# Performance work log

Measured on AMD Instinct MI355X. Metric: run time of the kernel, lower is better.

## Reference

```python
import jax, jax.numpy as jnp
import numpy as np

N_NODES = 50000
N_EDGES = 800000
NFEAT = 128
NHID = 64  # gc1: NFEAT -> 2*NHID, gc2: 2*NHID -> NHID


def setup_inputs() -> dict:
    key = jax.random.key(0)
    k1, k2, k3, k4, k5 = jax.random.split(key, 5)
    feat = jax.random.normal(k1, (N_NODES, NFEAT), dtype=jnp.float32)
    src = jax.random.randint(k2, (N_EDGES,), 0, N_NODES, dtype=jnp.int32)
    dst = jax.random.randint(k3, (N_EDGES,), 0, N_NODES, dtype=jnp.int32)
    # GraphConv weights: (in_feats, out_feats), xavier-like scale
    W1 = jax.random.normal(k4, (NFEAT, 2 * NHID), dtype=jnp.float32) / np.sqrt(NFEAT)
    b1 = jnp.zeros((2 * NHID,), dtype=jnp.float32)
    W2 = jax.random.normal(k5, (2 * NHID, NHID), dtype=jnp.float32) / np.sqrt(2 * NHID)
    b2 = jnp.zeros((NHID,), dtype=jnp.float32)
    return {"feat": feat, "src": src, "dst": dst, "W1": W1, "b1": b1, "W2": W2, "b2": b2}


def _graph_conv(feat, src, dst, W, b):
    """DGL GraphConv, norm='both', allow_zero_in_degree=True.
    h = D_in^{-1/2} A (D_out^{-1/2} x) W + b, with degrees clamped to >= 1.
    Applies W before aggregation when in_feats > out_feats (saves bandwidth)."""
    N = feat.shape[0]
    ones = jnp.ones(src.shape[0], dtype=feat.dtype)
    deg_out = jnp.clip(jax.ops.segment_sum(ones, src, num_segments=N), 1.0)
    deg_in = jnp.clip(jax.ops.segment_sum(ones, dst, num_segments=N), 1.0)
    h = feat * (deg_out ** -0.5)[:, None]
    mult_first = W.shape[0] > W.shape[1]
    if mult_first:
        h = h @ W
    agg = jax.ops.segment_sum(h[src], dst, num_segments=N)  # [N, d]
    if not mult_first:
        agg = agg @ W
    return agg * (deg_in ** -0.5)[:, None] + b


def reference(feat, src, dst, W1, b1, W2, b2):
    x = jax.nn.relu(_graph_conv(feat, src, dst, W1, b1))
    # dropout is inactive in eval mode (F.dropout training=False)
    x = _graph_conv(x, src, dst, W2, b2)
    return jax.nn.log_softmax(x, axis=1)
```

## Files before the change

kernel.cpp:

```cpp
#include <hip/hip_runtime.h>
#include <math.h>


constexpr int NF   = 128;
constexpr int NH   = 64;
constexpr int CAP  = 48;
constexpr int EPB  = 4096;
constexpr int BCAP = 8192;
constexpr int NBKMAX = 256;
constexpr int CASTB = 192;

typedef unsigned int uint;
typedef unsigned short ushort_t;
typedef __attribute__((ext_vector_type(8))) short short8;
typedef __attribute__((ext_vector_type(4))) float f32x4;

__device__ __forceinline__ float bflo(uint u) { return __uint_as_float(u << 16); }
__device__ __forceinline__ float bfhi(uint u) { return __uint_as_float(u & 0xffff0000u); }
__device__ __forceinline__ uint packbf(float a, float b) {
    uint ua = __float_as_uint(a), ub = __float_as_uint(b);
    uint ra = (ua + 0x7fffu + ((ua >> 16) & 1u)) >> 16;
    uint rb = (ub + 0x7fffu + ((ub >> 16) & 1u)) >> 16;
    return ra | (rb << 16);
}
__device__ __forceinline__ ushort_t bf16u(float f) {
    uint u = __float_as_uint(f);
    return (ushort_t)((u + 0x7fffu + ((u >> 16) & 1u)) >> 16);
}
__device__ __forceinline__ short8 as_short8(uint4 u) {
    union { uint4 u; short8 s; } x; x.u = u; return x.s;
}

__global__ __launch_bounds__(1024) void partition_kernel(
        const int* __restrict__ src, const int* __restrict__ dst,
        uint* __restrict__ pairs_g, ushort_t* __restrict__ srcb_g,
        int* __restrict__ dcur, int* __restrict__ scur,
        const float* __restrict__ W1, const float* __restrict__ W2,
        uint* __restrict__ W1p, uint* __restrict__ W2p,
        const float* __restrict__ feat, uint* __restrict__ featb,
        int E, int nbk, int nchunk, int N) {
    if (blockIdx.x >= nchunk) {
        int xb = blockIdx.x - nchunk;
        if (xb < 12) {
            int i = xb * 1024 + threadIdx.x;
            if (i < 8192) {
                int jp = i & 3, g = (i >> 2) & 3, n = (i >> 4) & 127, kk = i >> 11;
                int k = kk * 32 + g * 8 + jp * 2;
                W1p[i] = packbf(W1[k * 128 + n], W1[(k + 1) * 128 + n]);
            } else if (i < 12288) {
                int j = i - 8192;
                int jp = j & 3, g = (j >> 2) & 3, n = (j >> 4) & 63, kk = j >> 10;
                int k = kk * 32 + g * 8 + jp * 2;
                W2p[j] = packbf(W2[k * 64 + n], W2[(k + 1) * 64 + n]);
            }
        } else {
            int items = N * 16;
            for (int k = (xb - 12) * 1024 + threadIdx.x; k < items; k += CASTB * 1024) {
                int r = k >> 4, ch = k & 15;
                const float4* f4 = (const float4*)(feat + (size_t)r * NF + ch * 8);
                float4 a = f4[0], c = f4[1];
                uint4 o;
                o.x = packbf(a.x, a.y);
                o.y = packbf(a.z, a.w);
                o.z = packbf(c.x, c.y);
                o.w = packbf(c.z, c.w);
                *(uint4*)(featb + (size_t)r * 64 + ch * 4) = o;
            }
        }
        return;
    }
    __shared__ uint     pl[EPB];
    __shared__ ushort_t sl[EPB];
    __shared__ int dh[NBKMAX], sh[NBKMAX];
    __shared__ int doff[NBKMAX], soff[NBKMAX];
    __shared__ int dbase[NBKMAX], sbase[NBKMAX];
    __shared__ int dpos[NBKMAX], spos[NBKMAX];
    int tid = threadIdx.x;
    int e0 = blockIdx.x * EPB;
    int ecnt = min(EPB, E - e0);
    int ecnt4 = ecnt >> 2;
    bool own = tid < ecnt4;
    int4 sR = make_int4(0, 0, 0, 0), dR = make_int4(0, 0, 0, 0);
    if (own) {
        sR = ((const int4*)(src + e0))[tid];
        dR = ((const int4*)(dst + e0))[tid];
    }

    for (int b = tid; b < nbk; b += 1024) { dh[b] = 0; sh[b] = 0; }
    __syncthreads();
    if (own) {
        atomicAdd(&dh[dR.x >> 8], 1); atomicAdd(&dh[dR.y >> 8], 1);
        atomicAdd(&dh[dR.z >> 8], 1); atomicAdd(&dh[dR.w >> 8], 1);
        atomicAdd(&sh[sR.x >> 8], 1); atomicAdd(&sh[sR.y >> 8], 1);
        atomicAdd(&sh[sR.z >> 8], 1); atomicAdd(&sh[sR.w >> 8], 1);
    }
    for (int i = ecnt4 * 4 + tid; i < ecnt; i += 1024) {
        atomicAdd(&dh[dst[e0 + i] >> 8], 1);
        atomicAdd(&sh[src[e0 + i] >> 8], 1);
    }
    __syncthreads();
    if (tid < 128) {
        int wv = tid >> 6, l = tid & 63, b0 = l * 4;
        const int* h = wv ? sh : dh;
        int* of      = wv ? soff : doff;
        int v0 = (b0     < nbk) ? h[b0]     : 0;
        int v1 = (b0 + 1 < nbk) ? h[b0 + 1] : 0;
        int v2 = (b0 + 2 < nbk) ? h[b0 + 2] : 0;
        int v3 = (b0 + 3 < nbk) ? h[b0 + 3] : 0;
        int lsum = v0 + v1 + v2 + v3;
        int sc = lsum;
        #pragma unroll
        for (int off = 1; off < 64; off <<= 1) {
            int t = __shfl_up(sc, off, 64);
            if (l >= off) sc += t;
        }
        int excl = sc - lsum;
        if (b0     < nbk) of[b0]     = excl;
        if (b0 + 1 < nbk) of[b0 + 1] = excl + v0;
        if (b0 + 2 < nbk) of[b0 + 2] = excl + v0 + v1;
        if (b0 + 3 < nbk) of[b0 + 3] = excl + v0 + v1 + v2;
    }
    for (int b = tid; b < nbk; b += 1024) {
        dbase[b] = atomicAdd(&dcur[b], dh[b]);
        sbase[b] = atomicAdd(&scur[b], sh[b]);
    }
    __syncthreads();
    for (int b = tid; b < nbk; b += 1024) { dpos[b] = doff[b]; spos[b] = soff[b]; }
    __syncthreads();
    if (own) {
        #pragma unroll
        for (int j = 0; j < 4; ++j) {
            int sj = (j == 0) ? sR.x : (j == 1) ? sR.y : (j == 2) ? sR.z : sR.w;
            int dj = (j == 0) ? dR.x : (j == 1) ? dR.y : (j == 2) ? dR.z : dR.w;
            int p = atomicAdd(&dpos[dj >> 8], 1);
            pl[p] = ((uint)sj << 16) | (uint)dj;
            int q = atomicAdd(&spos[sj >> 8], 1);
            sl[q] = (ushort_t)sj;
        }
    }
    for (int i = ecnt4 * 4 + tid; i < ecnt; i += 1024) {
        int s = src[e0 + i], d = dst[e0 + i];
        int p = atomicAdd(&dpos[d >> 8], 1);
        pl[p] = ((uint)s << 16) | (uint)d;
        int q = atomicAdd(&spos[s >> 8], 1);
        sl[q] = (ushort_t)s;
    }
    __syncthreads();
    if (own) {
        uint4 e4 = *(const uint4*)&pl[tid * 4];
        ushort4 s4 = *(const ushort4*)&sl[tid * 4];
        #pragma unroll
        for (int j = 0; j < 4; ++j) {
            uint e = (j == 0) ? e4.x : (j == 1) ? e4.y : (j == 2) ? e4.z : e4.w;
            int i = tid * 4 + j;
            int b = (int)((e & 0xffffu) >> 8);
            int gp = dbase[b] + (i - doff[b]);
            if (gp < BCAP) pairs_g[(size_t)b * BCAP + gp] = e;
            ushort_t sv = (j == 0) ? s4.x : (j == 1) ? s4.y : (j == 2) ? s4.z : s4.w;
            int b2 = (int)(sv >> 8);
            int gq = sbase[b2] + (i - soff[b2]);
            if (gq < BCAP) srcb_g[(size_t)b2 * BCAP + gq] = sv;
        }
    }
    for (int i = ecnt4 * 4 + tid; i < ecnt; i += 1024) {
        uint e = pl[i];
        int b = (int)((e & 0xffffu) >> 8);
        int gp = dbase[b] + (i - doff[b]);
        if (gp < BCAP) pairs_g[(size_t)b * BCAP + gp] = e;
        ushort_t sv = sl[i];
        int b2 = (int)(sv >> 8);
        int gq = sbase[b2] + (i - soff[b2]);
        if (gq < BCAP) srcb_g[(size_t)b2 * BCAP + gq] = sv;
    }
}

__global__ __launch_bounds__(1024) void bin_kernel(
        const uint* __restrict__ pairs_g, const ushort_t* __restrict__ srcb_g,
        const int* __restrict__ dcur, const int* __restrict__ scur,
        ushort_t* __restrict__ slots, int* __restrict__ lens,
        float* __restrict__ s_in, float* __restrict__ s_out, int N) {
    __shared__ ushort_t slots_l[256 * CAP];
    __shared__ int cin[256], cout[256];
    int tid = threadIdx.x;
    int b = blockIdx.x;
    int lo = b << 8;
    for (int r = tid; r < 256; r += 1024) { cin[r] = 0; cout[r] = 0; }
    __syncthreads();
    int dn = min(dcur[b], BCAP);
    for (int i = tid; i < dn; i += 1024) {
        uint e = pairs_g[(size_t)b * BCAP + i];
        int r = (int)(e & 255u);
        int p = atomicAdd(&cin[r], 1);
        if (p < CAP) slots_l[r * CAP + p] = (ushort_t)(e >> 16);
    }
    int sn = min(scur[b], BCAP);
    for (int i = tid; i < sn; i += 1024)
        atomicAdd(&cout[(int)srcb_g[(size_t)b * BCAP + i] - lo], 1);
    __syncthreads();
    int nrow = min(256, N - lo);
    {
        const uint4* sl4 = (const uint4*)slots_l;
        uint4* gs4 = (uint4*)(slots + (size_t)lo * CAP);
        int lim4 = nrow * (CAP / 8);
        for (int k = tid; k < 256 * CAP / 8; k += 1024)
            if (k < lim4) gs4[k] = sl4[k];
    }
    for (int r = tid; r < nrow; r += 1024) {
        int node = lo + r;
        int ci = cin[r];
        lens[node]  = min(ci, CAP);
        s_in[node]  = rsqrtf((float)max(ci, 1));
        s_out[node] = rsqrtf((float)max(cout[r], 1));
    }
}

__global__ __launch_bounds__(256) void agg1_kernel(const uint* __restrict__ featb,
        const int* __restrict__ lens, const ushort_t* __restrict__ slots,
        const float* __restrict__ s_out, uint* __restrict__ agg1b, int N) {
    int wave = threadIdx.x >> 6;
    int lane = threadIdx.x & 63;
    int q   = lane >> 4;
    int sub = lane & 15;
    int node = blockIdx.x * 4 + wave;
    if (node >= N) return;
    int beg = node * CAP;
    int len = lens[node];
    float acc[8] = {0.f, 0.f, 0.f, 0.f, 0.f, 0.f, 0.f, 0.f};
    if (len > 0) {
        int li = min(lane, len - 1);
        int sidx = (int)slots[beg + li];
        int quads = (len + 3) >> 2;
        #pragma unroll 4
        for (int k = 0; k < quads; ++k) {
            int e = 4 * k + q;
            int s = __shfl(sidx, e, 64);
            if (e < len) {
                float so = s_out[s];
                uint4 v = *(const uint4*)(featb + (size_t)s * 64 + sub * 4);
                acc[0] = fmaf(so, bflo(v.x), acc[0]);
                acc[1] = fmaf(so, bfhi(v.x), acc[1]);
                acc[2] = fmaf(so, bflo(v.y), acc[2]);
                acc[3] = fmaf(so, bfhi(v.y), acc[3]);
                acc[4] = fmaf(so, bflo(v.z), acc[4]);
                acc[5] = fmaf(so, bfhi(v.z), acc[5]);
                acc[6] = fmaf(so, bflo(v.w), acc[6]);
                acc[7] = fmaf(so, bfhi(v.w), acc[7]);
            }
        }
    }
    #pragma unroll
    for (int j = 0; j < 8; ++j) {
        acc[j] += __shfl_xor(acc[j], 32, 64);
        acc[j] += __shfl_xor(acc[j], 16, 64);
    }
    if (q == 0) {
        uint4 o;
        o.x = packbf(acc[0], acc[1]);
        o.y = packbf(acc[2], acc[3]);
        o.z = packbf(acc[4], acc[5]);
        o.w = packbf(acc[6], acc[7]);
        *(uint4*)(agg1b + (size_t)node * 64 + sub * 4) = o;
    }
}

__global__ __launch_bounds__(256) void fused_gemm_kernel(
        const uint* __restrict__ agg1b, const uint* __restrict__ W1p,
        const float* __restrict__ b1, const uint* __restrict__ W2p,
        const float* __restrict__ s_in, const float* __restrict__ s_out,
        uint* __restrict__ h2b, int N) {
    __shared__ ushort_t x1t[64][136];
    __shared__ float sin_l[64], sout_l[64];
    int t = threadIdx.x;
    int base = blockIdx.x * 64;
    int w    = t >> 6;
    int lane = t & 63;
    int c = lane & 15;
    int g = lane >> 4;

    if (t < 64)       sin_l[t]        = (base + t < N) ? s_in[base + t] : 0.f;
    else if (t < 128) sout_l[t - 64]  = (base + t - 64 < N) ? s_out[base + t - 64] : 0.f;
    __syncthreads();

    f32x4 zero = {0.f, 0.f, 0.f, 0.f};
    f32x4 c1[4][2];
    #pragma unroll
    for (int mt = 0; mt < 4; ++mt) { c1[mt][0] = zero; c1[mt][1] = zero; }
    #pragma unroll
    for (int kk = 0; kk < 4; ++kk) {
        short8 bf[2];
        #pragma unroll
        for (int ntl = 0; ntl < 2; ++ntl) {
            int n = (2 * w + ntl) * 16 + c;
            bf[ntl] = as_short8(*(const uint4*)(W1p + (size_t)kk * 2048 + n * 16 + g * 4));
        }
        #pragma unroll
        for (int mt = 0; mt < 4; ++mt) {
            int row = base + mt * 16 + c;
            short8 af = as_short8(*(const uint4*)(agg1b + (size_t)row * 64 + kk * 16 + g * 4));
            c1[mt][0] = __builtin_amdgcn_mfma_f32_16x16x32_bf16(af, bf[0], c1[mt][0], 0, 0, 0);
            c1[mt][1] = __builtin_amdgcn_mfma_f32_16x16x32_bf16(af, bf[1], c1[mt][1], 0, 0, 0);
        }
    }
    float bias0 = b1[(2 * w) * 16 + c];
    float bias1 = b1[(2 * w + 1) * 16 + c];
    #pragma unroll
    for (int mt = 0; mt < 4; ++mt) {
        #pragma unroll
        for (int r = 0; r < 4; ++r) {
            int rl = mt * 16 + g * 4 + r;
            float si = sin_l[rl], so = sout_l[rl];
            x1t[rl][(2 * w) * 16 + c]     = bf16u(fmaxf(fmaf(si, c1[mt][0][r], bias0), 0.f) * so);
            x1t[rl][(2 * w + 1) * 16 + c] = bf16u(fmaxf(fmaf(si, c1[mt][1][r], bias1), 0.f) * so);
        }
    }
    __syncthreads();

    f32x4 c2[4];
    #pragma unroll
    for (int mt = 0; mt < 4; ++mt) c2[mt] = zero;
    #pragma unroll
    for (int kk = 0; kk < 4; ++kk) {
        int n = w * 16 + c;
        short8 bf2 = as_short8(*(const uint4*)(W2p + (size_t)kk * 1024 + n * 16 + g * 4));
        #pragma unroll
        for (int mt = 0; mt < 4; ++mt) {
            short8 af = *(const short8*)&x1t[mt * 16 + c][kk * 32 + g * 8];
            c2[mt] = __builtin_amdgcn_mfma_f32_16x16x32_bf16(af, bf2, c2[mt], 0, 0, 0);
        }
    }
    __syncthreads();

    ushort_t* h2t = &x1t[0][0];
    #pragma unroll
    for (int mt = 0; mt < 4; ++mt) {
        #pragma unroll
        for (int r = 0; r < 4; ++r) {
            int rl = mt * 16 + g * 4 + r;
            h2t[rl * 72 + w * 16 + c] = bf16u(c2[mt][r]);
        }
    }
    __syncthreads();
    int row = t >> 2, ch = t & 3;
    if (base + row < N) {
        uint4 v0 = *(const uint4*)(h2t + row * 72 + ch * 16);
        uint4 v1 = *(const uint4*)(h2t + row * 72 + ch * 16 + 8);
        *(uint4*)(h2b + (size_t)(base + row) * 32 + ch * 8)     = v0;
        *(uint4*)(h2b + (size_t)(base + row) * 32 + ch * 8 + 4) = v1;
    }
}

__global__ __launch_bounds__(256) void agg2_softmax_kernel(const uint* __restrict__ h2b,
        const int* __restrict__ lens, const ushort_t* __restrict__ slots,
        const float* __restrict__ s_in, const float* __restrict__ b2,
        float* __restrict__ out, int N) {
    int wave = threadIdx.x >> 6;
    int lane = threadIdx.x & 63;
    int oct = lane >> 3;
    int sub = lane & 7;
    int node = blockIdx.x * 4 + wave;
    if (node >= N) return;
    int beg = node * CAP;
    int len = lens[node];
    float acc[8] = {0.f, 0.f, 0.f, 0.f, 0.f, 0.f, 0.f, 0.f};
    if (len > 0) {
        int li = min(lane, len - 1);
        int sidx = (int)slots[beg + li];
        int octs = (len + 7) >> 3;
        #pragma unroll 4
        for (int k = 0; k < octs; ++k) {
            int e = 8 * k + oct;
            int s = __shfl(sidx, e, 64);
            if (e < len) {
                uint4 v = *(const uint4*)(h2b + (size_t)s * 32 + sub * 4);
                acc[0] += bflo(v.x); acc[1] += bfhi(v.x);
                acc[2] += bflo(v.y); acc[3] += bfhi(v.y);
                acc[4] += bflo(v.z); acc[5] += bfhi(v.z);
                acc[6] += bflo(v.w); acc[7] += bfhi(v.w);
            }
        }
    }
    #pragma unroll
    for (int j = 0; j < 8; ++j) {
        acc[j] += __shfl_xor(acc[j], 32, 64);
        acc[j] += __shfl_xor(acc[j], 16, 64);
        acc[j] += __shfl_xor(acc[j], 8, 64);
    }
    float si = s_in[node];
    float4 bb0 = *(const float4*)(b2 + sub * 8);
    float4 bb1 = *(const float4*)(b2 + sub * 8 + 4);
    float v[8];
    v[0] = fmaf(acc[0], si, bb0.x); v[1] = fmaf(acc[1], si, bb0.y);
    v[2] = fmaf(acc[2], si, bb0.z); v[3] = fmaf(acc[3], si, bb0.w);
    v[4] = fmaf(acc[4], si, bb1.x); v[5] = fmaf(acc[5], si, bb1.y);
    v[6] = fmaf(acc[6], si, bb1.z); v[7] = fmaf(acc[7], si, bb1.w);

    float m = v[0];
    #pragma unroll
    for (int j = 1; j < 8; ++j) m = fmaxf(m, v[j]);
    m = fmaxf(m, __shfl_xor(m, 4, 64));
    m = fmaxf(m, __shfl_xor(m, 2, 64));
    m = fmaxf(m, __shfl_xor(m, 1, 64));
    float s8 = 0.f;
    #pragma unroll
    for (int j = 0; j < 8; ++j) s8 += expf(v[j] - m);
    s8 += __shfl_xor(s8, 4, 64);
    s8 += __shfl_xor(s8, 2, 64);
    s8 += __shfl_xor(s8, 1, 64);
    float ls = m + logf(s8);
    if (oct == 0) {
        float4 o0 = make_float4(v[0] - ls, v[1] - ls, v[2] - ls, v[3] - ls);
        float4 o1 = make_float4(v[4] - ls, v[5] - ls, v[6] - ls, v[7] - ls);
        *(float4*)(out + (size_t)node * NH + sub * 8)     = o0;
        *(float4*)(out + (size_t)node * NH + sub * 8 + 4) = o1;
    }
}

extern "C" void kernel_launch(void* const* d_in, const int* in_sizes, int n_in,
                              void* d_out, int out_size, void* d_ws, size_t ws_size,
                              hipStream_t stream) {
    const float* feat = (const float*)d_in[0];
    const int*   src  = (const int*)d_in[1];
    const int*   dst  = (const int*)d_in[2];
    const float* W1   = (const float*)d_in[3];
    const float* b1   = (const float*)d_in[4];
    const float* W2   = (const float*)d_in[5];
    const float* b2   = (const float*)d_in[6];
    float* out = (float*)d_out;

    int N = in_sizes[0] / NF;
    int E = in_sizes[1];
    int nbk = (N + 255) >> 8;
    int nchunk = (E + EPB - 1) / EPB;
    int Npad = (N + 63) & ~63;

    char* p = (char*)d_ws;
    auto alloc = [&](size_t bytes) -> char* {
        char* q = p;
        p += (bytes + 255) & ~(size_t)255;
        return q;
    };
    int*      dcur  = (int*)alloc((size_t)nbk * 4);
    int*      scur  = (int*)alloc((size_t)nbk * 4);
    uint*     pairs = (uint*)alloc((size_t)nbk * BCAP * 4);
    ushort_t* srcb  = (ushort_t*)alloc((size_t)nbk * BCAP * 2);
    ushort_t* slots = (ushort_t*)alloc((size_t)N * CAP * 2);
    int*      lens  = (int*)alloc((size_t)N * 4);
    float*    s_out = (float*)alloc((size_t)N * 4);
    float*    s_in  = (float*)alloc((size_t)N * 4);
    uint*     featb = (uint*)alloc((size_t)N * 64 * 4);
    uint*     agg1b = (uint*)alloc((size_t)Npad * 64 * 4);
    uint*     W1p   = (uint*)alloc(8192 * 4);
    uint*     W2p   = (uint*)alloc(4096 * 4);
    uint*     h2b   = (uint*)alloc((size_t)N * 32 * 4);

    size_t cur_span = (size_t)((char*)scur - (char*)dcur) + (size_t)nbk * 4;
    hipMemsetAsync(dcur, 0, cur_span, stream);

    partition_kernel<<<nchunk + 12 + CASTB, 1024, 0, stream>>>(
        src, dst, pairs, srcb, dcur, scur, W1, W2, W1p, W2p, feat, featb,
        E, nbk, nchunk, N);
    bin_kernel<<<nbk, 1024, 0, stream>>>(pairs, srcb, dcur, scur,
                                         slots, lens, s_in, s_out, N);
    agg1_kernel<<<(N + 3) / 4, 256, 0, stream>>>(featb, lens, slots, s_out, agg1b, N);
    fused_gemm_kernel<<<(N + 63) / 64, 256, 0, stream>>>(agg1b, W1p, b1, W2p, s_in, s_out, h2b, N);
    agg2_softmax_kernel<<<(N + 3) / 4, 256, 0, stream>>>(h2b, lens, slots, s_in, b2, out, N);
}
```

Baseline: 170.6 us.

## Apply W1 before aggregation in partition side-blocks and fuse agg1 with W2 GEMM

Moves the first-layer W1 matmul ahead of aggregation: the feature-cast side blocks of the partition kernel now run a bf16 MFMA on each 64-row tile and write feat·W1 instead of plain bf16 features. The aggregation kernel then applies the degree scaling, bias and ReLU, and runs the small W2 MFMA on 16-node tiles. This removes the separate agg1b buffer and the fused_gemm launch. Weight packing and the cursor zeroing (previously a memset) move into a small prep kernel. This is valid because (D_out^{-1/2}x)W aggregated equals aggregating then multiplying. The cost is more bf16 rounding of intermediate results and heavier side blocks running alongside the partition work.

```diff
diff --git a/kernel.cpp b/kernel.cpp
--- a/kernel.cpp
+++ b/kernel.cpp
@@ -8,7 +8,7 @@
 constexpr int EPB  = 4096;
 constexpr int BCAP = 8192;
 constexpr int NBKMAX = 256;
-constexpr int CASTB = 192;
+constexpr int FWB  = 180;
 
 typedef unsigned int uint;
 typedef unsigned short ushort_t;
@@ -31,41 +31,83 @@
     union { uint4 u; short8 s; } x; x.u = u; return x.s;
 }
 
+__global__ __launch_bounds__(1024) void prep_kernel(
+        const float* __restrict__ W1, const float* __restrict__ W2,
+        uint* __restrict__ W1p, uint* __restrict__ W2p,
+        int* __restrict__ dcur, int* __restrict__ scur, int nbk) {
+    int i = blockIdx.x * 1024 + threadIdx.x;
+    if (i < 8192) {
+        int jp = i & 3, g = (i >> 2) & 3, n = (i >> 4) & 127, kk = i >> 11;
+        int k = kk * 32 + g * 8 + jp * 2;
+        W1p[i] = packbf(W1[k * 128 + n], W1[(k + 1) * 128 + n]);
+    } else if (i < 12288) {
+        int j = i - 8192;
+        int jp = j & 3, g = (j >> 2) & 3, n = (j >> 4) & 63, kk = j >> 10;
+        int k = kk * 32 + g * 8 + jp * 2;
+        W2p[j] = packbf(W2[k * 64 + n], W2[(k + 1) * 64 + n]);
+    } else {
+        int z = i - 12288;
+        if (z < nbk) dcur[z] = 0;
+        else if (z < 2 * nbk) scur[z - nbk] = 0;
+    }
+}
+
 __global__ __launch_bounds__(1024) void partition_kernel(
         const int* __restrict__ src, const int* __restrict__ dst,
         uint* __restrict__ pairs_g, ushort_t* __restrict__ srcb_g,
         int* __restrict__ dcur, int* __restrict__ scur,
-        const float* __restrict__ W1, const float* __restrict__ W2,
-        uint* __restrict__ W1p, uint* __restrict__ W2p,
-        const float* __restrict__ feat, uint* __restrict__ featb,
+        const uint* __restrict__ W1p,
+        const float* __restrict__ feat, uint* __restrict__ featW,
         int E, int nbk, int nchunk, int N) {
     if (blockIdx.x >= nchunk) {
+        __shared__ ushort_t xt[64][136];
         int xb = blockIdx.x - nchunk;
-        if (xb < 12) {
-            int i = xb * 1024 + threadIdx.x;
-            if (i < 8192) {
-                int jp = i & 3, g = (i >> 2) & 3, n = (i >> 4) & 127, kk = i >> 11;
-                int k = kk * 32 + g * 8 + jp * 2;
-                W1p[i] = packbf(W1[k * 128 + n], W1[(k + 1) * 128 + n]);
-            } else if (i < 12288) {
-                int j = i - 8192;
-                int jp = j & 3, g = (j >> 2) & 3, n = (j >> 4) & 63, kk = j >> 10;
-                int k = kk * 32 + g * 8 + jp * 2;
-                W2p[j] = packbf(W2[k * 64 + n], W2[(k + 1) * 64 + n]);
-            }
-        } else {
-            int items = N * 16;
-            for (int k = (xb - 12) * 1024 + threadIdx.x; k < items; k += CASTB * 1024) {
-                int r = k >> 4, ch = k & 15;
-                const float4* f4 = (const float4*)(feat + (size_t)r * NF + ch * 8);
-                float4 a = f4[0], c = f4[1];
-                uint4 o;
-                o.x = packbf(a.x, a.y);
-                o.y = packbf(a.z, a.w);
-                o.z = packbf(c.x, c.y);
-                o.w = packbf(c.z, c.w);
-                *(uint4*)(featb + (size_t)r * 64 + ch * 4) = o;
-            }
+        int tid = threadIdx.x;
+        int w = tid >> 6, lane = tid & 63, c = lane & 15, g = lane >> 4;
+        int mt = w & 3, np = w >> 2;
+        int sr = tid >> 4, f0 = (tid & 15) * 8;
+        int ntile = (N + 63) >> 6;
+        f32x4 zero = {0.f, 0.f, 0.f, 0.f};
+        for (int tile = xb; tile < ntile; tile += FWB) {
+            int tb = tile << 6;
+            {
+                int row = tb + sr;
+                uint4 o = make_uint4(0, 0, 0, 0);
+                if (row < N) {
+                    const float4* f4 = (const float4*)(feat + (size_t)row * NF + f0);
+                    float4 a = f4[0], cc = f4[1];
+                    o.x = packbf(a.x, a.y);  o.y = packbf(a.z, a.w);
+                    o.z = packbf(cc.x, cc.y); o.w = packbf(cc.z, cc.w);
+                }
+                *(uint4*)&xt[sr][f0] = o;
+            }
+            __syncthreads();
+            f32x4 c1[2]; c1[0] = zero; c1[1] = zero;
+            #pragma unroll
+            for (int kk = 0; kk < 4; ++kk) {
+                short8 af = *(const short8*)&xt[mt * 16 + c][kk * 32 + g * 8];
+                #pragma unroll
+                for (int ntl = 0; ntl < 2; ++ntl) {
+                    int n = (np * 2 + ntl) * 16 + c;
+                    short8 bf = as_short8(*(const uint4*)(W1p + (size_t)kk * 2048 + n * 16 + g * 4));
+                    c1[ntl] = __builtin_amdgcn_mfma_f32_16x16x32_bf16(af, bf, c1[ntl], 0, 0, 0);
+                }
+            }
+            __syncthreads();
+            #pragma unroll
+            for (int ntl = 0; ntl < 2; ++ntl) {
+                #pragma unroll
+                for (int rr = 0; rr < 4; ++rr)
+                    xt[mt * 16 + g * 4 + rr][(np * 2 + ntl) * 16 + c] = bf16u(c1[ntl][rr]);
+            }
+            __syncthreads();
+            {
+                int row = tid >> 4, u0 = (tid & 15) * 4;
+                if (tb + row < N)
+                    *(uint4*)(featW + (size_t)(tb + row) * 64 + u0) =
+                        *(const uint4*)((const uint*)&xt[0][0] + row * 68 + u0);
+            }
+            __syncthreads();
         }
         return;
     }
@@ -214,138 +256,96 @@
     }
 }
 
-__global__ __launch_bounds__(256) void agg1_kernel(const uint* __restrict__ featb,
+__global__ __launch_bounds__(1024) void agg1_fused_kernel(
+        const uint* __restrict__ featW,
         const int* __restrict__ lens, const ushort_t* __restrict__ slots,
-        const float* __restrict__ s_out, uint* __restrict__ agg1b, int N) {
-    int wave = threadIdx.x >> 6;
-    int lane = threadIdx.x & 63;
-    int q   = lane >> 4;
-    int sub = lane & 15;
-    int node = blockIdx.x * 4 + wave;
-    if (node >= N) return;
-    int beg = node * CAP;
-    int len = lens[node];
+        const float* __restrict__ s_in, const float* __restrict__ s_out,
+        const float* __restrict__ b1, const uint* __restrict__ W2p,
+        uint* __restrict__ h2b, int N) {
+    __shared__ ushort_t x1t[16][136];
+    __shared__ ushort_t h2t[16][72];
+    int tid  = threadIdx.x;
+    int wv   = tid >> 6;
+    int lane = tid & 63;
+    int q    = lane >> 4;
+    int sub  = lane & 15;
+    int base = blockIdx.x * 16;
+    int node = base + wv;
+
     float acc[8] = {0.f, 0.f, 0.f, 0.f, 0.f, 0.f, 0.f, 0.f};
-    if (len > 0) {
-        int li = min(lane, len - 1);
-        int sidx = (int)slots[beg + li];
-        int quads = (len + 3) >> 2;
-        #pragma unroll 4
-        for (int k = 0; k < quads; ++k) {
-            int e = 4 * k + q;
-            int s = __shfl(sidx, e, 64);
-            if (e < len) {
-                float so = s_out[s];
-                uint4 v = *(const uint4*)(featb + (size_t)s * 64 + sub * 4);
-                acc[0] = fmaf(so, bflo(v.x), acc[0]);
-                acc[1] = fmaf(so, bfhi(v.x), acc[1]);
-                acc[2] = fmaf(so, bflo(v.y), acc[2]);
-                acc[3] = fmaf(so, bfhi(v.y), acc[3]);
-                acc[4] = fmaf(so, bflo(v.z), acc[4]);
-                acc[5] = fmaf(so, bfhi(v.z), acc[5]);
-                acc[6] = fmaf(so, bflo(v.w), acc[6]);
-                acc[7] = fmaf(so, bfhi(v.w), acc[7]);
-            }
-        }
-    }
-    #pragma unroll
-    for (int j = 0; j < 8; ++j) {
-        acc[j] += __shfl_xor(acc[j], 32, 64);
-        acc[j] += __shfl_xor(acc[j], 16, 64);
-    }
-    if (q == 0) {
-        uint4 o;
-        o.x = packbf(acc[0], acc[1]);
-        o.y = packbf(acc[2], acc[3]);
-        o.z = packbf(acc[4], acc[5]);
-        o.w = packbf(acc[6], acc[7]);
-        *(uint4*)(agg1b + (size_t)node * 64 + sub * 4) = o;
-    }
-}
-
-__global__ __launch_bounds__(256) void fused_gemm_kernel(
-        const uint* __restrict__ agg1b, const uint* __restrict__ W1p,
-        const float* __restrict__ b1, const uint* __restrict__ W2p,
-        const float* __restrict__ s_in, const float* __restrict__ s_out,
-        uint* __restrict__ h2b, int N) {
-    __shared__ ushort_t x1t[64][136];
-    __shared__ float sin_l[64], sout_l[64];
-    int t = threadIdx.x;
-    int base = blockIdx.x * 64;
-    int w    = t >> 6;
-    int lane = t & 63;
-    int c = lane & 15;
-    int g = lane >> 4;
-
-    if (t < 64)       sin_l[t]        = (base + t < N) ? s_in[base + t] : 0.f;
-    else if (t < 128) sout_l[t - 64]  = (base + t - 64 < N) ? s_out[base + t - 64] : 0.f;
-    __syncthreads();
-
-    f32x4 zero = {0.f, 0.f, 0.f, 0.f};
-    f32x4 c1[4][2];
-    #pragma unroll
-    for (int mt = 0; mt < 4; ++mt) { c1[mt][0] = zero; c1[mt][1] = zero; }
-    #pragma unroll
-    for (int kk = 0; kk < 4; ++kk) {
-        short8 bf[2];
-        #pragma unroll
-        for (int ntl = 0; ntl < 2; ++ntl) {
-            int n = (2 * w + ntl) * 16 + c;
-            bf[ntl] = as_short8(*(const uint4*)(W1p + (size_t)kk * 2048 + n * 16 + g * 4));
-        }
-        #pragma unroll
-        for (int mt = 0; mt < 4; ++mt) {
-            int row = base + mt * 16 + c;
-            short8 af = as_short8(*(const uint4*)(agg1b + (size_t)row * 64 + kk * 16 + g * 4));
-            c1[mt][0] = __builtin_amdgcn_mfma_f32_16x16x32_bf16(af, bf[0], c1[mt][0], 0, 0, 0);
-            c1[mt][1] = __builtin_amdgcn_mfma_f32_16x16x32_bf16(af, bf[1], c1[mt][1], 0, 0, 0);
-        }
-    }
-    float bias0 = b1[(2 * w) * 16 + c];
-    float bias1 = b1[(2 * w + 1) * 16 + c];
-    #pragma unroll
-    for (int mt = 0; mt < 4; ++mt) {
-        #pragma unroll
-        for (int r = 0; r < 4; ++r) {
-            int rl = mt * 16 + g * 4 + r;
-            float si = sin_l[rl], so = sout_l[rl];
-            x1t[rl][(2 * w) * 16 + c]     = bf16u(fmaxf(fmaf(si, c1[mt][0][r], bias0), 0.f) * so);
-            x1t[rl][(2 * w + 1) * 16 + c] = bf16u(fmaxf(fmaf(si, c1[mt][1][r], bias1), 0.f) * so);
-        }
-    }
-    __syncthreads();
-
-    f32x4 c2[4];
-    #pragma unroll
-    for (int mt = 0; mt < 4; ++mt) c2[mt] = zero;
-    #pragma unroll
-    for (int kk = 0; kk < 4; ++kk) {
-        int n = w * 16 + c;
-        short8 bf2 = as_short8(*(const uint4*)(W2p + (size_t)kk * 1024 + n * 16 + g * 4));
-        #pragma unroll
-        for (int mt = 0; mt < 4; ++mt) {
-            short8 af = *(const short8*)&x1t[mt * 16 + c][kk * 32 + g * 8];
-            c2[mt] = __builtin_amdgcn_mfma_f32_16x16x32_bf16(af, bf2, c2[mt], 0, 0, 0);
-        }
-    }
-    __syncthreads();
-
-    ushort_t* h2t = &x1t[0][0];
-    #pragma unroll
-    for (int mt = 0; mt < 4; ++mt) {
-        #pragma unroll
-        for (int r = 0; r < 4; ++r) {
-            int rl = mt * 16 + g * 4 + r;
-            h2t[rl * 72 + w * 16 + c] = bf16u(c2[mt][r]);
-        }
-    }
-    __syncthreads();
-    int row = t >> 2, ch = t & 3;
-    if (base + row < N) {
-        uint4 v0 = *(const uint4*)(h2t + row * 72 + ch * 16);
-        uint4 v1 = *(const uint4*)(h2t + row * 72 + ch * 16 + 8);
-        *(uint4*)(h2b + (size_t)(base + row) * 32 + ch * 8)     = v0;
-        *(uint4*)(h2b + (size_t)(base + row) * 32 + ch * 8 + 4) = v1;
+    if (node < N) {
+        int beg = node * CAP;
+        int len = lens[node];
+        if (len > 0) {
+            int li = min(lane, len - 1);
+            int sidx = (int)slots[beg + li];
+            int quads = (len + 3) >> 2;
+            #pragma unroll 4
+            for (int k = 0; k < quads; ++k) {
+                int e = 4 * k + q;
+                int s = __shfl(sidx, e, 64);
+                if (e < len) {
+                    float so = s_out[s];
+                    uint4 v = *(const uint4*)(featW + (size_t)s * 64 + sub * 4);
+                    acc[0] = fmaf(so, bflo(v.x), acc[0]);
+                    acc[1] = fmaf(so, bfhi(v.x), acc[1]);
+                    acc[2] = fmaf(so, bflo(v.y), acc[2]);
+                    acc[3] = fmaf(so, bfhi(v.y), acc[3]);
+                    acc[4] = fmaf(so, bflo(v.z), acc[4]);
+                    acc[5] = fmaf(so, bfhi(v.z), acc[5]);
+                    acc[6] = fmaf(so, bflo(v.w), acc[6]);
+                    acc[7] = fmaf(so, bfhi(v.w), acc[7]);
+                }
+            }
+        }
+        #pragma unroll
+        for (int j = 0; j < 8; ++j) {
+            acc[j] += __shfl_xor(acc[j], 32, 64);
+            acc[j] += __shfl_xor(acc[j], 16, 64);
+        }
+        if (q == 0) {
+            float si = s_in[node], so = s_out[node];
+            float4 bb0 = *(const float4*)(b1 + sub * 8);
+            float4 bb1 = *(const float4*)(b1 + sub * 8 + 4);
+            float x0 = fmaxf(fmaf(si, acc[0], bb0.x), 0.f) * so;
+            float x1 = fmaxf(fmaf(si, acc[1], bb0.y), 0.f) * so;
+            float x2 = fmaxf(fmaf(si, acc[2], bb0.z), 0.f) * so;
+            float x3 = fmaxf(fmaf(si, acc[3], bb0.w), 0.f) * so;
+            float x4 = fmaxf(fmaf(si, acc[4], bb1.x), 0.f) * so;
+            float x5 = fmaxf(fmaf(si, acc[5], bb1.y), 0.f) * so;
+            float x6 = fmaxf(fmaf(si, acc[6], bb1.z), 0.f) * so;
+            float x7 = fmaxf(fmaf(si, acc[7], bb1.w), 0.f) * so;
+            uint4 o;
+            o.x = packbf(x0, x1); o.y = packbf(x2, x3);
+            o.z = packbf(x4, x5); o.w = packbf(x6, x7);
+            *(uint4*)&x1t[wv][sub * 8] = o;
+        }
+    } else if (q == 0) {
+        uint4 z = make_uint4(0, 0, 0, 0);
+        *(uint4*)&x1t[wv][sub * 8] = z;
+    }
+    __syncthreads();
+
+    if (wv < 4) {
+        f32x4 c2 = {0.f, 0.f, 0.f, 0.f};
+        int n = wv * 16 + sub;
+        #pragma unroll
+        for (int kk = 0; kk < 4; ++kk) {
+            short8 bf2 = as_short8(*(const uint4*)(W2p + (size_t)kk * 1024 + n * 16 + q * 4));
+            short8 af = *(const short8*)&x1t[sub][kk * 32 + q * 8];
+            c2 = __builtin_amdgcn_mfma_f32_16x16x32_bf16(af, bf2, c2, 0, 0, 0);
+        }
+        #pragma unroll
+        for (int r = 0; r < 4; ++r)
+            h2t[q * 4 + r][wv * 16 + sub] = bf16u(c2[r]);
+    }
+    __syncthreads();
+
+    if (tid < 128) {
+        int row = tid >> 3, u0 = (tid & 7) * 4;
+        if (base + row < N)
+            *(uint4*)(h2b + (size_t)(base + row) * 32 + u0) =
+                *(const uint4*)((const uint*)&h2t[row][0] + u0);
     }
 }
 
@@ -431,7 +431,6 @@
     int E = in_sizes[1];
     int nbk = (N + 255) >> 8;
     int nchunk = (E + EPB - 1) / EPB;
-    int Npad = (N + 63) & ~63;
 
     char* p = (char*)d_ws;
     auto alloc = [&](size_t bytes) -> char* {
@@ -447,21 +446,17 @@
     int*      lens  = (int*)alloc((size_t)N * 4);
     float*    s_out = (float*)alloc((size_t)N * 4);
     float*    s_in  = (float*)alloc((size_t)N * 4);
-    uint*     featb = (uint*)alloc((size_t)N * 64 * 4);
-    uint*     agg1b = (uint*)alloc((size_t)Npad * 64 * 4);
+    uint*     featW = (uint*)alloc((size_t)N * 64 * 4);
     uint*     W1p   = (uint*)alloc(8192 * 4);
     uint*     W2p   = (uint*)alloc(4096 * 4);
     uint*     h2b   = (uint*)alloc((size_t)N * 32 * 4);
 
-    size_t cur_span = (size_t)((char*)scur - (char*)dcur) + (size_t)nbk * 4;
-    hipMemsetAsync(dcur, 0, cur_span, stream);
-
-    partition_kernel<<<nchunk + 12 + CASTB, 1024, 0, stream>>>(
-        src, dst, pairs, srcb, dcur, scur, W1, W2, W1p, W2p, feat, featb,
-        E, nbk, nchunk, N);
+    prep_kernel<<<13, 1024, 0, stream>>>(W1, W2, W1p, W2p, dcur, scur, nbk);
+    partition_kernel<<<nchunk + FWB, 1024, 0, stream>>>(
+        src, dst, pairs, srcb, dcur, scur, W1p, feat, featW, E, nbk, nchunk, N);
     bin_kernel<<<nbk, 1024, 0, stream>>>(pairs, srcb, dcur, scur,
                                          slots, lens, s_in, s_out, N);
-    agg1_kernel<<<(N + 3) / 4, 256, 0, stream>>>(featb, lens, slots, s_out, agg1b, N);
-    fused_gemm_kernel<<<(N + 63) / 64, 256, 0, stream>>>(agg1b, W1p, b1, W2p, s_in, s_out, h2b, N);
+    agg1_fused_kernel<<<(N + 15) / 16, 1024, 0, stream>>>(
+        featW, lens, slots, s_in, s_out, b1, W2p, h2b, N);
     agg2_softmax_kernel<<<(N + 3) / 4, 256, 0, stream>>>(h2b, lens, slots, s_in, b2, out, N);
 }
```

After: 169.9 us. About the same (-0.4%).
